# Optimization experiments

Measured on AMD Instinct MI355X. Metric: run time of the kernel, lower is better.

The kernel has to match this reference:

```python
import jax, jax.numpy as jnp
import numpy as np

D_MODEL = 1024
NUM_HEADS = 16
HDIM = D_MODEL // NUM_HEADS
THETA = 10000.0


def setup_inputs() -> dict:
    key = jax.random.key(0)
    ks = jax.random.split(key, 5)
    bs, seq = 4, 2048
    std = np.sqrt(2.0 / (D_MODEL + D_MODEL))
    def w(k):
        # trunc_normal approximated by clipped normal (same distribution family)
        return jnp.clip(std * jax.random.normal(k, (D_MODEL, D_MODEL), jnp.float32), -3 * std, 3 * std)
    return {
        "x": jax.random.normal(ks[0], (bs, seq, D_MODEL), jnp.float32),
        "Wq": w(ks[1]), "Wk": w(ks[2]), "Wv": w(ks[3]), "Wo": w(ks[4]),
        "token_positions": jnp.arange(seq, dtype=jnp.int64),
    }


def _rope(x, token_positions):
    # x: (bs, H, S, hdim); rotate even/odd interleaved pairs
    inv_freq = THETA ** (-2.0 * jnp.arange(HDIM // 2, dtype=jnp.float32) / HDIM)
    freqs = token_positions.astype(jnp.float32)[:, None] * inv_freq[None, :]  # (S, hdim/2)
    cos, sin = jnp.cos(freqs), jnp.sin(freqs)
    x_even, x_odd = x[..., 0::2], x[..., 1::2]
    out_even = x_even * cos - x_odd * sin
    out_odd = x_odd * cos + x_even * sin
    # interleave back: stack on new last axis then reshape
    return jnp.stack([out_even, out_odd], axis=-1).reshape(x.shape)


def reference(x, Wq, Wk, Wv, Wo, token_positions):
    bs, seq, _ = x.shape
    q = (x @ Wq.T).reshape(bs, seq, NUM_HEADS, HDIM).transpose(0, 2, 1, 3)
    k = (x @ Wk.T).reshape(bs, seq, NUM_HEADS, HDIM).transpose(0, 2, 1, 3)
    v = (x @ Wv.T).reshape(bs, seq, NUM_HEADS, HDIM).transpose(0, 2, 1, 3)
    q = _rope(q, token_positions)
    k = _rope(k, token_positions)
    scores = jnp.einsum("bhsd,bhtd->bhst", q, k) / jnp.sqrt(jnp.float32(HDIM))
    mask = jnp.tril(jnp.ones((seq, seq), dtype=bool))
    scores = jnp.where(mask, scores, -jnp.inf)
    attn = jax.nn.softmax(scores, axis=-1)
    out = jnp.einsum("bhst,bhtd->bhsd", attn, v)
    out = out.transpose(0, 2, 1, 3).reshape(bs, seq, D_MODEL)
    return out @ Wo.T
```

## Files before the change

kernel.cpp:

```cpp
#include <hip/hip_runtime.h>
#include <hip/hip_fp16.h>

typedef _Float16 half8 __attribute__((ext_vector_type(8)));
typedef _Float16 half4 __attribute__((ext_vector_type(4)));
typedef _Float16 half2v __attribute__((ext_vector_type(2)));
typedef float f32x4 __attribute__((ext_vector_type(4)));
typedef float f32x8v __attribute__((ext_vector_type(8)));
typedef float f32x16 __attribute__((ext_vector_type(16)));

#define SEQ   2048
#define DM    1024
#define NH    16
#define HD    64
#define BSZ   4

#if __has_builtin(__builtin_amdgcn_exp2f)
#define EXP2(x) __builtin_amdgcn_exp2f(x)
#else
#define EXP2(x) exp2f(x)
#endif

#define QSCALE 0.1803368801f
#define ROPE_C 0.41524101186f

__device__ __forceinline__ void gload16(const void* g, void* l) {
  __builtin_amdgcn_global_load_lds((const __attribute__((address_space(1))) void*)g,
                                   (__attribute__((address_space(3))) void*)l,
                                   16, 0, 0);
}

__global__ void cvt4(const float* __restrict__ src, _Float16* __restrict__ dst, int n4) {
  int i = blockIdx.x * blockDim.x + threadIdx.x;
  if (i < n4) {
    float4 v = ((const float4*)src)[i];
    half4 o = { (_Float16)v.x, (_Float16)v.y, (_Float16)v.z, (_Float16)v.w };
    ((half4*)dst)[i] = o;
  }
}

__global__ void cvtW(const float* __restrict__ s0, const float* __restrict__ s1,
                     const float* __restrict__ s2, const float* __restrict__ s3,
                     _Float16* __restrict__ dqkv, _Float16* __restrict__ dO) {
  const int y = blockIdx.y;
  const float* src = (y == 0) ? s0 : (y == 1) ? s1 : (y == 2) ? s2 : s3;
  _Float16* dst = (y < 3) ? (dqkv + (long)y * (1u << 20)) : dO;
  int i = blockIdx.x * blockDim.x + threadIdx.x;
  float4 v = ((const float4*)src)[i];
  half4 o = { (_Float16)v.x, (_Float16)v.y, (_Float16)v.z, (_Float16)v.w };
  ((half4*)dst)[i] = o;
}

template<int MODE>
__global__ __launch_bounds__(256)
void gemm_hk(const _Float16* __restrict__ A, const _Float16* __restrict__ B,
             _Float16* __restrict__ oQ, _Float16* __restrict__ oK,
             _Float16* __restrict__ oVt, float* __restrict__ oF,
             const int* __restrict__ tp) {
  __shared__ _Float16 As[2][128*32];
  __shared__ _Float16 Bs[2][128*32];
  const int tid  = threadIdx.x;
  const int wid  = tid >> 6, lane = tid & 63;
  const int wm   = wid >> 1, wn = wid & 1;
  const int fr   = lane & 15, fg = lane >> 4;
  const long m0  = (long)blockIdx.x * 128;
  const long n0  = (long)blockIdx.y * 128;
  const int sg    = (lane & 7) ^ ((lane >> 3) & 7);
  const int srowl = 2*(lane >> 3) + (sg >> 2);
  const int scol  = (sg & 3) * 8;
  const _Float16* ga0 = A + (m0 + wid*32 + srowl) * 1024 + scol;
  const _Float16* gb0 = B + (n0 + wid*32 + srowl) * 1024 + scol;
  const int lofs = wid*32*32;

  f32x4 acc[4][4] = {};

  auto ldfrag = [&](const char* base, int R) -> half8 {
    const int r = R & 31, r2 = r >> 1;
    return *(const half8*)(base + (R >> 5)*2048 + r2*128 +
                           (((((r & 1) << 2) | fg) ^ (r2 & 7)) << 4));
  };

  gload16(ga0,           &As[0][lofs]);
  gload16(ga0 + 16*1024, &As[0][lofs + 16*32]);
  gload16(gb0,           &Bs[0][lofs]);
  gload16(gb0 + 16*1024, &Bs[0][lofs + 16*32]);
  __syncthreads();

  int cur = 0;
  for (int k0 = 0; k0 < 1024; k0 += 32) {
    if (k0 + 32 < 1024) {
      gload16(ga0 + k0 + 32,           &As[cur^1][lofs]);
      gload16(ga0 + k0 + 32 + 16*1024, &As[cur^1][lofs + 16*32]);
      gload16(gb0 + k0 + 32,           &Bs[cur^1][lofs]);
      gload16(gb0 + k0 + 32 + 16*1024, &Bs[cur^1][lofs + 16*32]);
    }
    const char* Ab = (const char*)&As[cur][0];
    const char* Bb = (const char*)&Bs[cur][0];
    half8 af[4], bf[4];
#pragma unroll
    for (int i = 0; i < 4; ++i) {
      af[i] = ldfrag(Ab, wm*64 + i*16 + fr);
      bf[i] = ldfrag(Bb, wn*64 + i*16 + fr);
    }
    __builtin_amdgcn_s_setprio(1);
#pragma unroll
    for (int i = 0; i < 4; ++i)
#pragma unroll
      for (int j = 0; j < 4; ++j)
        acc[i][j] = __builtin_amdgcn_mfma_f32_16x16x32_f16(af[i], bf[j], acc[i][j], 0, 0, 0);
    __builtin_amdgcn_s_setprio(0);
    __syncthreads();
    cur ^= 1;
  }

  if (MODE == 0) {
    const int which = (int)(n0 >> 10);
    const int nloc0 = ((int)n0 & 1023) + wn*64;
    const bool odd = fr & 1;
#pragma unroll
    for (int i = 0; i < 4; ++i) {
      const long r0 = m0 + wm*64 + i*16 + fg*4;
      const int  bb = (int)(r0 >> 11);
      const int  s  = (int)(r0 & 2047);
#pragma unroll
      for (int j = 0; j < 4; ++j) {
        const int nl = nloc0 + j*16 + fr;
        const int h  = nl >> 6, d = nl & 63;
        const long bh = (long)(bb*NH + h);
        if (which == 2) {
          half4 pk = { (_Float16)acc[i][j][0], (_Float16)acc[i][j][1],
                       (_Float16)acc[i][j][2], (_Float16)acc[i][j][3] };
          *(half4*)&oVt[(bh*HD + d)*SEQ + s] = pk;
        } else {
          const float inv = exp2f(-ROPE_C * (float)(d >> 1));
#pragma unroll
          for (int r = 0; r < 4; ++r) {
            const float v = acc[i][j][r];
            const float p = __shfl_xor(v, 1);
            float sn, cs;
            __sincosf((float)tp[s + r] * inv, &sn, &cs);
            const float out = odd ? (v*cs + p*sn) : (v*cs - p*sn);
            if (which == 0)
              oQ[(bh*SEQ + s + r)*HD + d] = (_Float16)(out * QSCALE);
            else
              oK[(bh*SEQ + s + r)*HD + d] = (_Float16)out;
          }
        }
      }
    }
  } else {
#pragma unroll
    for (int i = 0; i < 4; ++i) {
      const long r0 = m0 + wm*64 + i*16 + fg*4;
#pragma unroll
      for (int j = 0; j < 4; ++j) {
        const long col = n0 + wn*64 + j*16 + fr;
#pragma unroll
        for (int r = 0; r < 4; ++r)
          oF[(r0 + r)*DM + col] = acc[i][j][r];
      }
    }
  }
}

__global__ __launch_bounds__(256, 2)
void fattn(const _Float16* __restrict__ Q, const _Float16* __restrict__ K,
           const _Float16* __restrict__ Vt, _Float16* __restrict__ O) {
  __shared__ _Float16 Ks[2][64*64];
  __shared__ _Float16 Vs[2][64*64];
  const int tid = threadIdx.x, wid = tid >> 6, lane = tid & 63;
  const int q31 = lane & 31, hi = lane >> 5;
  const int qp  = (q31 & 19) | ((q31 & 4) << 1) | ((q31 & 8) >> 1);
  const int bh = blockIdx.x, b = bh >> 4, h = bh & 15;
  const int y = blockIdx.y;
  const int qs_[2] = { (15 - y)*128 + wid*32, y*128 + wid*32 };
  const _Float16* Qb = Q + (long)bh * SEQ * HD;
  const _Float16* Kb = K + (long)bh * SEQ * HD;
  const _Float16* Vb = Vt + (long)bh * HD * SEQ;

  half8 qf[2][4];
#pragma unroll
  for (int s = 0; s < 2; ++s)
#pragma unroll
    for (int c = 0; c < 4; ++c)
      qf[s][c] = *(const half8*)&Qb[(qs_[s] + q31)*HD + c*16 + hi*8];

  f32x16 oacc[2][2] = {};
  float m_s[2] = { -1e30f, -1e30f }, l_s[2] = { 0.f, 0.f };

  const int srow = lane >> 3;
  const int sc16 = (lane & 7) ^ srow;
  const int r1 = wid*16 + srow, r2 = r1 + 8;

  const int nt = (15 - y)*2 + 2;

  gload16(Kb + (long)r1*HD + sc16*8, &Ks[0][(wid*16)*64]);
  gload16(Kb + (long)r2*HD + sc16*8, &Ks[0][(wid*16 + 8)*64]);
  gload16(Vb + (long)r1*SEQ + sc16*8, &Vs[0][(wid*16)*64]);
  gload16(Vb + (long)r2*SEQ + sc16*8, &Vs[0][(wid*16 + 8)*64]);
  __syncthreads();

  int cur = 0;
  for (int t = 0; t < nt; ++t) {
    const int kv0 = t * 64;

    if (t + 1 < nt) {
      const int nkv = kv0 + 64;
      gload16(Kb + (long)(nkv + r1)*HD + sc16*8, &Ks[cur^1][(wid*16)*64]);
      gload16(Kb + (long)(nkv + r2)*HD + sc16*8, &Ks[cur^1][(wid*16 + 8)*64]);
      gload16(Vb + (long)r1*SEQ + nkv + sc16*8,  &Vs[cur^1][(wid*16)*64]);
      gload16(Vb + (long)r2*SEQ + nkv + sc16*8,  &Vs[cur^1][(wid*16 + 8)*64]);
    }

    const char* Kc = (const char*)&Ks[cur][0];
    const char* Vc = (const char*)&Vs[cur][0];

#pragma unroll
    for (int hh = 0; hh < 2; ++hh) {
      const int kvb = kv0 + 32*hh;
#pragma unroll
      for (int s = 0; s < 2; ++s) {
        const int qs0 = qs_[s];
        if (kvb > qs0 + 31) continue;

        f32x16 sa = {};
        __builtin_amdgcn_s_setprio(1);
#pragma unroll
        for (int c = 0; c < 4; ++c) {
          const int row = 32*hh + qp;
          const half8 kf = *(const half8*)(Kc + row*128 + ((c*32 + hi*16) ^ ((row & 7) << 4)));
          sa = __builtin_amdgcn_mfma_f32_32x32x16_f16(kf, qf[s][c], sa, 0, 0, 0);
        }
        __builtin_amdgcn_s_setprio(0);

        if (kvb + 31 > qs0) {
          const int thr = qs0 + q31 - kvb - 8*hi;
#pragma unroll
          for (int r = 0; r < 16; ++r) {
            const int cr = (r & 3) + 4*((r >> 2) & 1) + 16*(r >> 3);
            if (cr > thr) sa[r] = -1e30f;
          }
        }

        f32x8v mx8;
#pragma unroll
        for (int i = 0; i < 8; ++i) mx8[i] = fmaxf(sa[i], sa[i+8]);
        f32x4 mx4;
#pragma unroll
        for (int i = 0; i < 4; ++i) mx4[i] = fmaxf(mx8[i], mx8[i+4]);
        float pm = fmaxf(fmaxf(mx4[0], mx4[1]), fmaxf(mx4[2], mx4[3]));
        pm = fmaxf(pm, __shfl_xor(pm, 32));

        if (!__all(pm <= m_s[s] + 8.0f)) {
          const float mn = fmaxf(m_s[s], pm);
          const float fac = EXP2(m_s[s] - mn);
          m_s[s] = mn;
          l_s[s] *= fac;
          oacc[s][0] *= fac;
          oacc[s][1] *= fac;
        }
        const float mrow = m_s[s];

#pragma unroll
        for (int r = 0; r < 16; ++r) sa[r] = EXP2(sa[r] - mrow);

        f32x8v s8;
#pragma unroll
        for (int i = 0; i < 8; ++i) s8[i] = sa[i] + sa[i+8];
        f32x4 s4v;
#pragma unroll
        for (int i = 0; i < 4; ++i) s4v[i] = s8[i] + s8[i+4];
        float ps = (s4v[0] + s4v[1]) + (s4v[2] + s4v[3]);
        ps += __shfl_xor(ps, 32);
        l_s[s] += ps;

        half8 pf0, pf1;
#pragma unroll
        for (int g = 0; g < 4; ++g) {
          half2v t0 = (half2v)__builtin_amdgcn_cvt_pkrtz(sa[2*g],   sa[2*g+1]);
          half2v t1 = (half2v)__builtin_amdgcn_cvt_pkrtz(sa[8+2*g], sa[8+2*g+1]);
          pf0[2*g]   = t0[0];  pf0[2*g+1] = t0[1];
          pf1[2*g]   = t1[0];  pf1[2*g+1] = t1[1];
        }

        __builtin_amdgcn_s_setprio(1);
#pragma unroll
        for (int ks = 0; ks < 2; ++ks) {
          const half8 pf = ks ? pf1 : pf0;
#pragma unroll
          for (int nd = 0; nd < 2; ++nd) {
            const int row = nd*32 + q31;
            const half8 vf = *(const half8*)(Vc + row*128 +
                              ((hh*64 + ks*32 + hi*16) ^ ((row & 7) << 4)));
            oacc[s][nd] = __builtin_amdgcn_mfma_f32_32x32x16_f16(vf, pf, oacc[s][nd], 0, 0, 0);
          }
        }
        __builtin_amdgcn_s_setprio(0);
      }
    }

    __syncthreads();
    cur ^= 1;
  }

#pragma unroll
  for (int s = 0; s < 2; ++s) {
    const float rl = __builtin_amdgcn_rcpf(l_s[s]);
    _Float16* orow = O + ((long)b*SEQ + (qs_[s] + q31))*DM + h*64;
#pragma unroll
    for (int nd = 0; nd < 2; ++nd)
#pragma unroll
      for (int g = 0; g < 4; ++g) {
        half2v lo  = (half2v)__builtin_amdgcn_cvt_pkrtz(oacc[s][nd][4*g+0]*rl, oacc[s][nd][4*g+1]*rl);
        half2v hi2 = (half2v)__builtin_amdgcn_cvt_pkrtz(oacc[s][nd][4*g+2]*rl, oacc[s][nd][4*g+3]*rl);
        half4 o4 = __builtin_shufflevector(lo, hi2, 0, 1, 2, 3);
        *(half4*)&orow[nd*32 + g*8 + 4*hi] = o4;
      }
  }
}

extern "C" void kernel_launch(void* const* d_in, const int* in_sizes, int n_in,
                              void* d_out, int out_size, void* d_ws, size_t ws_size,
                              hipStream_t stream) {
  const float* x  = (const float*)d_in[0];
  const float* Wq = (const float*)d_in[1];
  const float* Wk = (const float*)d_in[2];
  const float* Wv = (const float*)d_in[3];
  const float* Wo = (const float*)d_in[4];
  const int*   tp = (const int*)d_in[5];
  float* out = (float*)d_out;

  char* ws = (char*)d_ws;
  _Float16* xh   = (_Float16*)(ws);
  _Float16* Wqkv = (_Float16*)(ws + (16u << 20));
  _Float16* Woh  = (_Float16*)(ws + (22u << 20));
  _Float16* Qb   = (_Float16*)(ws + (24u << 20));
  _Float16* Kb   = (_Float16*)(ws + (40u << 20));
  _Float16* Vtb  = (_Float16*)(ws + (56u << 20));
  _Float16* attn = (_Float16*)(ws + (72u << 20));

  cvt4<<<8192, 256, 0, stream>>>(x, xh, 2097152);
  cvtW<<<dim3(1024, 4), 256, 0, stream>>>(Wq, Wk, Wv, Wo, Wqkv, Woh);

  gemm_hk<0><<<dim3(64, 24), 256, 0, stream>>>(xh, Wqkv, Qb, Kb, Vtb, nullptr, tp);
  fattn<<<dim3(64, 8), 256, 0, stream>>>(Qb, Kb, Vtb, attn);
  gemm_hk<1><<<dim3(64, 8), 256, 0, stream>>>(attn, Woh, nullptr, nullptr, nullptr, out, nullptr);
}
```

Measured before the change: 168.8 us.

## Replace QKV GEMM with 256x256-tile, 8-wave ping-pong pipelined kernel

Introduces a new QKV projection GEMM using 256x256 output tiles, 512 threads, and a double-buffered LDS schedule. Barriers interleave async global-to-LDS loads with quarter-tile MFMA batches. The larger tile is meant to raise data reuse per block and hide load latency behind MFMA work. It leaves only 384 blocks at one block per CU, which risks underfilling the GPU and tail effects. The output-projection GEMM keeps the old 128x128 kernel under a new name.

```diff
diff --git a/kernel.cpp b/kernel.cpp
--- a/kernel.cpp
+++ b/kernel.cpp
@@ -50,12 +50,161 @@
   ((half4*)dst)[i] = o;
 }
 
-template<int MODE>
+__global__ __launch_bounds__(512, 1)
+void gemm8p(const _Float16* __restrict__ A, const _Float16* __restrict__ B,
+            _Float16* __restrict__ oQ, _Float16* __restrict__ oK,
+            _Float16* __restrict__ oVt, const int* __restrict__ tp) {
+  __shared__ _Float16 Ls[2][16384];
+  const int tid = threadIdx.x;
+  const int w = tid >> 6, lane = tid & 63;
+  const int wm = w >> 2, wnn = w & 3;
+  const int fr = lane & 15, fg = lane >> 4;
+  const long m0 = (long)blockIdx.x * 256;
+  const long n0 = (long)blockIdx.y * 256;
+
+  const int l3 = lane >> 3;
+  const int sg = (lane & 7) ^ l3;
+  const _Float16* pA = A + (m0 + 2*l3 + (sg >> 2))*1024 + (sg & 3)*8;
+  const _Float16* pB = B + (n0 + 2*l3 + (sg >> 2))*1024 + (sg & 3)*8;
+  char* lds0 = (char*)&Ls[0][0];
+
+  auto stA = [&](int b, int i, int k) {
+    gload16(pA + ((i*8 + w)*16)*1024 + k, lds0 + b*32768 + (i*8 + w)*1024);
+  };
+  auto stB = [&](int b, int i, int k) {
+    gload16(pB + ((i*8 + w)*16)*1024 + k, lds0 + b*32768 + 16384 + (i*8 + w)*1024);
+  };
+  auto ldfrag = [&](const char* bb, int R) -> half8 {
+    const int r = R & 31, r2 = r >> 1;
+    return *(const half8*)(bb + (R >> 5)*2048 + r2*128 +
+                           (((((r & 1) << 2) | fg) ^ (r2 & 7)) << 4));
+  };
+
+  f32x4 acc[8][4] = {};
+
+  stA(0, 0, 0);  stA(0, 1, 0);  stB(0, 0, 0);  stB(0, 1, 0);
+  stB(1, 0, 32); stB(1, 1, 32);
+  asm volatile("s_waitcnt vmcnt(2)" ::: "memory");
+  __builtin_amdgcn_s_barrier();
+
+  half8 af[4], bf[4];
+  const char* Ab0 = lds0;             const char* Bb0 = lds0 + 16384;
+  const char* Ab1 = lds0 + 32768;     const char* Bb1 = lds0 + 32768 + 16384;
+
+#define MFMA_Q(MB, NB)                                                        \
+  __builtin_amdgcn_s_setprio(1);                                              \
+  _Pragma("unroll")                                                           \
+  for (int mi = 0; mi < 4; ++mi)                                              \
+    _Pragma("unroll")                                                         \
+    for (int ni = 0; ni < 2; ++ni)                                            \
+      acc[MB + mi][NB + ni] =                                                 \
+        __builtin_amdgcn_mfma_f32_16x16x32_f16(af[mi], bf[NB + ni],           \
+                                               acc[MB + mi][NB + ni], 0, 0, 0);\
+  __builtin_amdgcn_s_setprio(0);
+
+  for (int it = 0; it < 16; ++it) {
+    const bool more = (it < 15);
+    const int kt1 = (2*it + 1) * 32, kt2 = (2*it + 2) * 32, kt3 = (2*it + 3) * 32;
+
+#pragma unroll
+    for (int mi = 0; mi < 4; ++mi) af[mi] = ldfrag(Ab0, wm*128 + mi*16 + fr);
+#pragma unroll
+    for (int ni = 0; ni < 2; ++ni) bf[ni] = ldfrag(Bb0, wnn*64 + ni*16 + fr);
+    stA(1, 0, kt1);
+    __builtin_amdgcn_s_barrier();
+    MFMA_Q(0, 0)
+    __builtin_amdgcn_s_barrier();
+
+#pragma unroll
+    for (int ni = 2; ni < 4; ++ni) bf[ni] = ldfrag(Bb0, wnn*64 + ni*16 + fr);
+    stA(1, 1, kt1);
+    __builtin_amdgcn_s_barrier();
+    MFMA_Q(0, 2)
+    __builtin_amdgcn_s_barrier();
+
+#pragma unroll
+    for (int mi = 0; mi < 4; ++mi) af[mi] = ldfrag(Ab0, wm*128 + (4 + mi)*16 + fr);
+    if (more) stB(0, 0, kt2);
+    __builtin_amdgcn_s_barrier();
+    MFMA_Q(4, 2)
+    __builtin_amdgcn_s_barrier();
+
+    if (more) { stB(0, 1, kt2); asm volatile("s_waitcnt vmcnt(2)" ::: "memory"); }
+    else      {                 asm volatile("s_waitcnt vmcnt(0)" ::: "memory"); }
+    __builtin_amdgcn_s_barrier();
+    MFMA_Q(4, 0)
+    __builtin_amdgcn_s_barrier();
+
+#pragma unroll
+    for (int mi = 0; mi < 4; ++mi) af[mi] = ldfrag(Ab1, wm*128 + mi*16 + fr);
+#pragma unroll
+    for (int ni = 0; ni < 2; ++ni) bf[ni] = ldfrag(Bb1, wnn*64 + ni*16 + fr);
+    if (more) stA(0, 0, kt2);
+    __builtin_amdgcn_s_barrier();
+    MFMA_Q(0, 0)
+    __builtin_amdgcn_s_barrier();
+
+#pragma unroll
+    for (int ni = 2; ni < 4; ++ni) bf[ni] = ldfrag(Bb1, wnn*64 + ni*16 + fr);
+    if (more) stA(0, 1, kt2);
+    __builtin_amdgcn_s_barrier();
+    MFMA_Q(0, 2)
+    __builtin_amdgcn_s_barrier();
+
+#pragma unroll
+    for (int mi = 0; mi < 4; ++mi) af[mi] = ldfrag(Ab1, wm*128 + (4 + mi)*16 + fr);
+    if (more) stB(1, 0, kt3);
+    __builtin_amdgcn_s_barrier();
+    MFMA_Q(4, 2)
+    __builtin_amdgcn_s_barrier();
+
+    if (more) { stB(1, 1, kt3); asm volatile("s_waitcnt vmcnt(2)" ::: "memory"); }
+    else      {                 asm volatile("s_waitcnt vmcnt(0)" ::: "memory"); }
+    __builtin_amdgcn_s_barrier();
+    MFMA_Q(4, 0)
+    __builtin_amdgcn_s_barrier();
+  }
+#undef MFMA_Q
+
+  const int which = (int)(n0 >> 10);
+  const int nloc0 = ((int)n0 & 1023) + wnn*64;
+  const bool odd = fr & 1;
+#pragma unroll
+  for (int mi = 0; mi < 8; ++mi) {
+    const long r0 = m0 + wm*128 + mi*16 + fg*4;
+    const int  bb = (int)(r0 >> 11);
+    const int  s  = (int)(r0 & 2047);
+#pragma unroll
+    for (int ni = 0; ni < 4; ++ni) {
+      const int nl = nloc0 + ni*16 + fr;
+      const int h  = nl >> 6, d = nl & 63;
+      const long bh = (long)(bb*NH + h);
+      if (which == 2) {
+        half4 pk = { (_Float16)acc[mi][ni][0], (_Float16)acc[mi][ni][1],
+                     (_Float16)acc[mi][ni][2], (_Float16)acc[mi][ni][3] };
+        *(half4*)&oVt[(bh*HD + d)*SEQ + s] = pk;
+      } else {
+        const float inv = exp2f(-ROPE_C * (float)(d >> 1));
+#pragma unroll
+        for (int r = 0; r < 4; ++r) {
+          const float v = acc[mi][ni][r];
+          const float p = __shfl_xor(v, 1);
+          float sn, cs;
+          __sincosf((float)tp[s + r] * inv, &sn, &cs);
+          const float out = odd ? (v*cs + p*sn) : (v*cs - p*sn);
+          if (which == 0)
+            oQ[(bh*SEQ + s + r)*HD + d] = (_Float16)(out * QSCALE);
+          else
+            oK[(bh*SEQ + s + r)*HD + d] = (_Float16)out;
+        }
+      }
+    }
+  }
+}
+
 __global__ __launch_bounds__(256)
-void gemm_hk(const _Float16* __restrict__ A, const _Float16* __restrict__ B,
-             _Float16* __restrict__ oQ, _Float16* __restrict__ oK,
-             _Float16* __restrict__ oVt, float* __restrict__ oF,
-             const int* __restrict__ tp) {
+void gemm_out(const _Float16* __restrict__ A, const _Float16* __restrict__ B,
+              float* __restrict__ oF) {
   __shared__ _Float16 As[2][128*32];
   __shared__ _Float16 Bs[2][128*32];
   const int tid  = threadIdx.x;
@@ -112,52 +261,15 @@
     cur ^= 1;
   }
 
-  if (MODE == 0) {
-    const int which = (int)(n0 >> 10);
-    const int nloc0 = ((int)n0 & 1023) + wn*64;
-    const bool odd = fr & 1;
-#pragma unroll
-    for (int i = 0; i < 4; ++i) {
-      const long r0 = m0 + wm*64 + i*16 + fg*4;
-      const int  bb = (int)(r0 >> 11);
-      const int  s  = (int)(r0 & 2047);
-#pragma unroll
-      for (int j = 0; j < 4; ++j) {
-        const int nl = nloc0 + j*16 + fr;
-        const int h  = nl >> 6, d = nl & 63;
-        const long bh = (long)(bb*NH + h);
-        if (which == 2) {
-          half4 pk = { (_Float16)acc[i][j][0], (_Float16)acc[i][j][1],
-                       (_Float16)acc[i][j][2], (_Float16)acc[i][j][3] };
-          *(half4*)&oVt[(bh*HD + d)*SEQ + s] = pk;
-        } else {
-          const float inv = exp2f(-ROPE_C * (float)(d >> 1));
-#pragma unroll
-          for (int r = 0; r < 4; ++r) {
-            const float v = acc[i][j][r];
-            const float p = __shfl_xor(v, 1);
-            float sn, cs;
-            __sincosf((float)tp[s + r] * inv, &sn, &cs);
-            const float out = odd ? (v*cs + p*sn) : (v*cs - p*sn);
-            if (which == 0)
-              oQ[(bh*SEQ + s + r)*HD + d] = (_Float16)(out * QSCALE);
-            else
-              oK[(bh*SEQ + s + r)*HD + d] = (_Float16)out;
-          }
-        }
-      }
-    }
-  } else {
-#pragma unroll
-    for (int i = 0; i < 4; ++i) {
-      const long r0 = m0 + wm*64 + i*16 + fg*4;
-#pragma unroll
-      for (int j = 0; j < 4; ++j) {
-        const long col = n0 + wn*64 + j*16 + fr;
-#pragma unroll
-        for (int r = 0; r < 4; ++r)
-          oF[(r0 + r)*DM + col] = acc[i][j][r];
-      }
+#pragma unroll
+  for (int i = 0; i < 4; ++i) {
+    const long r0 = m0 + wm*64 + i*16 + fg*4;
+#pragma unroll
+    for (int j = 0; j < 4; ++j) {
+      const long col = n0 + wn*64 + j*16 + fr;
+#pragma unroll
+      for (int r = 0; r < 4; ++r)
+        oF[(r0 + r)*DM + col] = acc[i][j][r];
     }
   }
 }
@@ -341,7 +453,7 @@
   cvt4<<<8192, 256, 0, stream>>>(x, xh, 2097152);
   cvtW<<<dim3(1024, 4), 256, 0, stream>>>(Wq, Wk, Wv, Wo, Wqkv, Woh);
 
-  gemm_hk<0><<<dim3(64, 24), 256, 0, stream>>>(xh, Wqkv, Qb, Kb, Vtb, nullptr, tp);
+  gemm8p<<<dim3(32, 12), 512, 0, stream>>>(xh, Wqkv, Qb, Kb, Vtb, tp);
   fattn<<<dim3(64, 8), 256, 0, stream>>>(Qb, Kb, Vtb, attn);
-  gemm_hk<1><<<dim3(64, 8), 256, 0, stream>>>(attn, Woh, nullptr, nullptr, nullptr, out, nullptr);
-}
+  gemm_out<<<dim3(64, 8), 256, 0, stream>>>(attn, Woh, out);
+}
```

Result: slower. 173.3 us (+2.6%).

## Process full 64-key tile per softmax step and share K/V fragments across both query strips

Applied to the files above, without the earlier changes.

Restructures the attention inner loop so QK^T is computed for both 32-key halves and both query strips before a single softmax over the whole 64-key tile. Each K and V fragment loaded from LDS is now reused for both query strips, and the online-softmax max/rescale runs once per 64 keys instead of once per 32. This cuts LDS reads and reduction/rescale overhead and exposes more independent MFMAs. In exchange it holds more accumulators live, which raises register pressure and may lower occupancy.

```diff
diff --git a/kernel.cpp b/kernel.cpp
--- a/kernel.cpp
+++ b/kernel.cpp
@@ -214,89 +214,107 @@
     const char* Kc = (const char*)&Ks[cur][0];
     const char* Vc = (const char*)&Vs[cur][0];
 
+    const bool act0 = (kv0 <= qs_[0] + 31);
+    const bool act1 = (kv0 <= qs_[1] + 31);
+
+    f32x16 sa[2][2] = {};
+    __builtin_amdgcn_s_setprio(1);
 #pragma unroll
     for (int hh = 0; hh < 2; ++hh) {
-      const int kvb = kv0 + 32*hh;
-#pragma unroll
-      for (int s = 0; s < 2; ++s) {
-        const int qs0 = qs_[s];
-        if (kvb > qs0 + 31) continue;
-
-        f32x16 sa = {};
-        __builtin_amdgcn_s_setprio(1);
-#pragma unroll
-        for (int c = 0; c < 4; ++c) {
-          const int row = 32*hh + qp;
-          const half8 kf = *(const half8*)(Kc + row*128 + ((c*32 + hi*16) ^ ((row & 7) << 4)));
-          sa = __builtin_amdgcn_mfma_f32_32x32x16_f16(kf, qf[s][c], sa, 0, 0, 0);
-        }
-        __builtin_amdgcn_s_setprio(0);
-
+      const int row = 32*hh + qp;
+#pragma unroll
+      for (int c = 0; c < 4; ++c) {
+        const half8 kf = *(const half8*)(Kc + row*128 + ((c*32 + hi*16) ^ ((row & 7) << 4)));
+        if (act0) sa[0][hh] = __builtin_amdgcn_mfma_f32_32x32x16_f16(kf, qf[0][c], sa[0][hh], 0, 0, 0);
+        if (act1) sa[1][hh] = __builtin_amdgcn_mfma_f32_32x32x16_f16(kf, qf[1][c], sa[1][hh], 0, 0, 0);
+      }
+    }
+    __builtin_amdgcn_s_setprio(0);
+
+    half8 pf[2][4];
+#pragma unroll
+    for (int s = 0; s < 2; ++s) {
+      if (s == 0 ? !act0 : !act1) continue;
+      const int qs0 = qs_[s];
+#pragma unroll
+      for (int hh = 0; hh < 2; ++hh) {
+        const int kvb = kv0 + 32*hh;
         if (kvb + 31 > qs0) {
           const int thr = qs0 + q31 - kvb - 8*hi;
 #pragma unroll
           for (int r = 0; r < 16; ++r) {
             const int cr = (r & 3) + 4*((r >> 2) & 1) + 16*(r >> 3);
-            if (cr > thr) sa[r] = -1e30f;
+            if (cr > thr) sa[s][hh][r] = -1e30f;
           }
         }
-
-        f32x8v mx8;
-#pragma unroll
-        for (int i = 0; i < 8; ++i) mx8[i] = fmaxf(sa[i], sa[i+8]);
-        f32x4 mx4;
-#pragma unroll
-        for (int i = 0; i < 4; ++i) mx4[i] = fmaxf(mx8[i], mx8[i+4]);
-        float pm = fmaxf(fmaxf(mx4[0], mx4[1]), fmaxf(mx4[2], mx4[3]));
-        pm = fmaxf(pm, __shfl_xor(pm, 32));
-
-        if (!__all(pm <= m_s[s] + 8.0f)) {
-          const float mn = fmaxf(m_s[s], pm);
-          const float fac = EXP2(m_s[s] - mn);
-          m_s[s] = mn;
-          l_s[s] *= fac;
-          oacc[s][0] *= fac;
-          oacc[s][1] *= fac;
-        }
-        const float mrow = m_s[s];
-
-#pragma unroll
-        for (int r = 0; r < 16; ++r) sa[r] = EXP2(sa[r] - mrow);
-
-        f32x8v s8;
-#pragma unroll
-        for (int i = 0; i < 8; ++i) s8[i] = sa[i] + sa[i+8];
-        f32x4 s4v;
-#pragma unroll
-        for (int i = 0; i < 4; ++i) s4v[i] = s8[i] + s8[i+4];
-        float ps = (s4v[0] + s4v[1]) + (s4v[2] + s4v[3]);
-        ps += __shfl_xor(ps, 32);
-        l_s[s] += ps;
-
-        half8 pf0, pf1;
-#pragma unroll
-        for (int g = 0; g < 4; ++g) {
-          half2v t0 = (half2v)__builtin_amdgcn_cvt_pkrtz(sa[2*g],   sa[2*g+1]);
-          half2v t1 = (half2v)__builtin_amdgcn_cvt_pkrtz(sa[8+2*g], sa[8+2*g+1]);
-          pf0[2*g]   = t0[0];  pf0[2*g+1] = t0[1];
-          pf1[2*g]   = t1[0];  pf1[2*g+1] = t1[1];
-        }
-
-        __builtin_amdgcn_s_setprio(1);
-#pragma unroll
-        for (int ks = 0; ks < 2; ++ks) {
-          const half8 pf = ks ? pf1 : pf0;
-#pragma unroll
-          for (int nd = 0; nd < 2; ++nd) {
-            const int row = nd*32 + q31;
-            const half8 vf = *(const half8*)(Vc + row*128 +
-                              ((hh*64 + ks*32 + hi*16) ^ ((row & 7) << 4)));
-            oacc[s][nd] = __builtin_amdgcn_mfma_f32_32x32x16_f16(vf, pf, oacc[s][nd], 0, 0, 0);
+      }
+
+      f32x16 m01;
+#pragma unroll
+      for (int i = 0; i < 16; ++i) m01[i] = fmaxf(sa[s][0][i], sa[s][1][i]);
+      f32x8v mx8;
+#pragma unroll
+      for (int i = 0; i < 8; ++i) mx8[i] = fmaxf(m01[i], m01[i+8]);
+      f32x4 mx4;
+#pragma unroll
+      for (int i = 0; i < 4; ++i) mx4[i] = fmaxf(mx8[i], mx8[i+4]);
+      float pm = fmaxf(fmaxf(mx4[0], mx4[1]), fmaxf(mx4[2], mx4[3]));
+      pm = fmaxf(pm, __shfl_xor(pm, 32));
+
+      if (!__all(pm <= m_s[s] + 8.0f)) {
+        const float mn = fmaxf(m_s[s], pm);
+        const float fac = EXP2(m_s[s] - mn);
+        m_s[s] = mn;
+        l_s[s] *= fac;
+        oacc[s][0] *= fac;
+        oacc[s][1] *= fac;
+      }
+      const float mrow = m_s[s];
+
+#pragma unroll
+      for (int hh = 0; hh < 2; ++hh)
+#pragma unroll
+        for (int r = 0; r < 16; ++r)
+          sa[s][hh][r] = EXP2(sa[s][hh][r] - mrow);
+
+      f32x16 s16;
+#pragma unroll
+      for (int i = 0; i < 16; ++i) s16[i] = sa[s][0][i] + sa[s][1][i];
+      f32x8v s8;
+#pragma unroll
+      for (int i = 0; i < 8; ++i) s8[i] = s16[i] + s16[i+8];
+      f32x4 s4v;
+#pragma unroll
+      for (int i = 0; i < 4; ++i) s4v[i] = s8[i] + s8[i+4];
+      float ps = (s4v[0] + s4v[1]) + (s4v[2] + s4v[3]);
+      ps += __shfl_xor(ps, 32);
+      l_s[s] += ps;
+
+#pragma unroll
+      for (int hh = 0; hh < 2; ++hh)
+#pragma unroll
+        for (int ks = 0; ks < 2; ++ks)
+#pragma unroll
+          for (int g = 0; g < 4; ++g) {
+            half2v tt = (half2v)__builtin_amdgcn_cvt_pkrtz(sa[s][hh][8*ks + 2*g],
+                                                           sa[s][hh][8*ks + 2*g + 1]);
+            pf[s][2*hh + ks][2*g]     = tt[0];
+            pf[s][2*hh + ks][2*g + 1] = tt[1];
           }
-        }
-        __builtin_amdgcn_s_setprio(0);
-      }
-    }
+    }
+
+    __builtin_amdgcn_s_setprio(1);
+#pragma unroll
+    for (int ks = 0; ks < 4; ++ks) {
+#pragma unroll
+      for (int nd = 0; nd < 2; ++nd) {
+        const int row = nd*32 + q31;
+        const half8 vf = *(const half8*)(Vc + row*128 + ((ks*32 + hi*16) ^ ((row & 7) << 4)));
+        if (act0) oacc[0][nd] = __builtin_amdgcn_mfma_f32_32x32x16_f16(vf, pf[0][ks], oacc[0][nd], 0, 0, 0);
+        if (act1) oacc[1][nd] = __builtin_amdgcn_mfma_f32_32x32x16_f16(vf, pf[1][ks], oacc[1][nd], 0, 0, 0);
+      }
+    }
+    __builtin_amdgcn_s_setprio(0);
 
     __syncthreads();
     cur ^= 1;
```

Result: slower. 177.0 us (+4.8%).
